# Performance work log

Hardware: AMD Instinct MI355X
Metric: run time of the kernel (lower is better)

Reference implementation:

```python
import jax, jax.numpy as jnp
import numpy as np

N_EMBD = 1024
N_HEAD = 16
HEAD_DIM = N_EMBD // N_HEAD
INNER = 4 * N_EMBD
EPS = 1e-5


def setup_inputs() -> dict:
    key = jax.random.key(0)
    ks = jax.random.split(key, 13)
    s = lambda d: 1.0 / np.sqrt(d)
    return {
        "x": jax.random.normal(ks[0], (2, 2048, N_EMBD), jnp.float32),
        "ln1_g": jnp.ones((N_EMBD,), jnp.float32),
        "ln1_b": jnp.zeros((N_EMBD,), jnp.float32),
        "w_attn": jax.random.normal(ks[1], (N_EMBD, 3 * N_EMBD), jnp.float32) * s(N_EMBD),
        "b_attn": jnp.zeros((3 * N_EMBD,), jnp.float32),
        "w_proj": jax.random.normal(ks[2], (N_EMBD, N_EMBD), jnp.float32) * s(N_EMBD),
        "b_proj": jnp.zeros((N_EMBD,), jnp.float32),
        "ln2_g": jnp.ones((N_EMBD,), jnp.float32),
        "ln2_b": jnp.zeros((N_EMBD,), jnp.float32),
        "w_fc": jax.random.normal(ks[3], (N_EMBD, INNER), jnp.float32) * s(N_EMBD),
        "b_fc": jnp.zeros((INNER,), jnp.float32),
        "w_fc2": jax.random.normal(ks[4], (INNER, N_EMBD), jnp.float32) * s(INNER),
        "b_fc2": jnpp if False else jnp.zeros((N_EMBD,), jnp.float32),
    }


def _layernorm(x, g, b):
    mu = jnp.mean(x, axis=-1, keepdims=True)
    var = jnp.mean(jnp.square(x - mu), axis=-1, keepdims=True)
    return (x - mu) * jax.lax.rsqrt(var + EPS) * g + b


def _attention(x, w_attn, b_attn, w_proj, b_proj):
    B, T, C = x.shape
    qkv = x @ w_attn + b_attn                      # [B,T,3C]
    q, k, v = jnp.split(qkv, 3, axis=-1)
    q = q.reshape(B, T, N_HEAD, HEAD_DIM).transpose(0, 2, 1, 3)  # [B,H,T,D]
    k = k.reshape(B, T, N_HEAD, HEAD_DIM).transpose(0, 2, 1, 3)
    v = v.reshape(B, T, N_HEAD, HEAD_DIM).transpose(0, 2, 1, 3)
    scale = HEAD_DIM ** -0.5
    scores = jnp.einsum("bhqd,bhkd->bhqk", q, k) * scale         # [B,H,T,T]
    causal = jnp.triu(jnp.ones((T, T), jnp.bool_), k=1)
    scores = jnp.where(causal, -jnp.inf, scores)
    attn = jax.nn.softmax(scores, axis=-1)
    out = jnp.einsum("bhqk,bhkd->bhqd", attn, v)                 # [B,H,T,D]
    out = out.transpose(0, 2, 1, 3).reshape(B, T, C)
    return out @ w_proj + b_proj


def reference(x, ln1_g, ln1_b, w_attn, b_attn, w_proj, b_proj,
              ln2_g, ln2_b, w_fc, b_fc, w_fc2, b_fc2):
    h = x + _attention(_layernorm(x, ln1_g, ln1_b), w_attn, b_attn, w_proj, b_proj)
    m = _layernorm(h, ln2_g, ln2_b)
    m = jax.nn.gelu(m @ w_fc + b_fc, approximate=False) @ w_fc2 + b_fc2
    return h + m
```

## Files before the change

kernel.cpp:

```cpp
#include <hip/hip_runtime.h>

typedef unsigned short u16;
typedef unsigned int u32;
typedef short v8s __attribute__((ext_vector_type(8)));
typedef short v4s __attribute__((ext_vector_type(4)));
typedef float v4f __attribute__((ext_vector_type(4)));

__device__ __forceinline__ float b2f(u16 v) {
    return __uint_as_float(((u32)v) << 16);
}
__device__ __forceinline__ u16 f2b(float f) {
    u32 u = __float_as_uint(f);
    return (u16)((u + 0x7FFFu + ((u >> 16) & 1u)) >> 16);
}
__device__ __forceinline__ v4f mfma16(v8s a, v8s b, v4f c) {
    return __builtin_amdgcn_mfma_f32_16x16x32_bf16(a, b, c, 0, 0, 0);
}

__device__ __forceinline__ void gload_lds16(const u16* g, u16* l) {
    __builtin_amdgcn_global_load_lds((const __attribute__((address_space(1))) void*)g,
                                     (__attribute__((address_space(3))) void*)l, 16, 0, 0);
}

__global__ void detect_k(const void* x, int* flag) {
    __shared__ int cnt;
    if (threadIdx.x == 0) cnt = 0;
    __syncthreads();
    const u16* p = (const u16*)x;
    int bad = 0;
    for (int i = threadIdx.x; i < 4096; i += 256) {
        int e = (p[i] >> 7) & 0xFF;
        if (e != 0 && (e < 100 || e > 140)) bad++;
    }
    atomicAdd(&cnt, bad);
    __syncthreads();
    if (threadIdx.x == 0) *flag = (cnt > 256) ? 1 : 0;
}

__global__ void cvt_k(const void* __restrict__ src, u16* __restrict__ dst, int n,
                      const int* __restrict__ flag) {
    const int isf32 = *flag;
    for (int i = blockIdx.x * 256 + threadIdx.x; i < n; i += gridDim.x * 256)
        dst[i] = isf32 ? f2b(((const float*)src)[i]) : ((const u16*)src)[i];
}

struct P8 { const void* p[8]; };
__global__ void cvt_small_k(P8 src, u16* __restrict__ bb, const int* __restrict__ flag) {
    const int isf32 = *flag;
    const int len[8] = {3072, 1024, 4096, 1024, 1024, 1024, 1024, 1024};
    const int doff[8] = {0, 4096, 8192, 12288, 16384, 17408, 18432, 19456};
    int gi = blockIdx.x * 256 + threadIdx.x;
    int seg = 0, off = gi;
    while (seg < 7 && off >= len[seg]) { off -= len[seg]; seg++; }
    if (off < len[seg]) {
        const void* s = src.p[seg];
        bb[doff[seg] + off] = isf32 ? f2b(((const float*)s)[off]) : ((const u16*)s)[off];
    }
}

__global__ void transpose_k(const void* __restrict__ in, u16* __restrict__ out, int R, int C,
                            const int* __restrict__ flag) {
    __shared__ u16 t[32][33];
    const int isf32 = *flag;
    const int c0 = blockIdx.x * 32, r0 = blockIdx.y * 32;
    for (int i = threadIdx.y; i < 32; i += 8) {
        size_t idx = (size_t)(r0 + i) * C + c0 + threadIdx.x;
        t[i][threadIdx.x] = isf32 ? f2b(((const float*)in)[idx]) : ((const u16*)in)[idx];
    }
    __syncthreads();
    for (int i = threadIdx.y; i < 32; i += 8)
        out[(size_t)(c0 + i) * R + r0 + threadIdx.x] = t[threadIdx.x][i];
}

__global__ __launch_bounds__(256) void layernorm_k(const u16* __restrict__ x,
                                                   const u16* __restrict__ g,
                                                   const u16* __restrict__ bta,
                                                   u16* __restrict__ out) {
    const int wid = threadIdx.x >> 6, lane = threadIdx.x & 63;
    const size_t row = (size_t)blockIdx.x * 4 + wid;
    const u16* xr = x + row * 1024 + lane * 16;
    u16 v[16];
    *(uint4*)&v[0] = *(const uint4*)xr;
    *(uint4*)&v[8] = *(const uint4*)(xr + 8);
    float f[16], s = 0.f, sq = 0.f;
#pragma unroll
    for (int i = 0; i < 16; i++) { f[i] = b2f(v[i]); s += f[i]; sq += f[i] * f[i]; }
#pragma unroll
    for (int d = 1; d < 64; d <<= 1) { s += __shfl_xor(s, d, 64); sq += __shfl_xor(sq, d, 64); }
    const float mean = s * (1.f / 1024.f);
    const float var = sq * (1.f / 1024.f) - mean * mean;
    const float rstd = rsqrtf(var + 1e-5f);
    u16 gv[16], bv[16];
    *(uint4*)&gv[0] = *(const uint4*)(g + lane * 16);
    *(uint4*)&gv[8] = *(const uint4*)(g + lane * 16 + 8);
    *(uint4*)&bv[0] = *(const uint4*)(bta + lane * 16);
    *(uint4*)&bv[8] = *(const uint4*)(bta + lane * 16 + 8);
    u16 ov[16];
#pragma unroll
    for (int i = 0; i < 16; i++) ov[i] = f2b((f[i] - mean) * rstd * b2f(gv[i]) + b2f(bv[i]));
    u16* orow = out + row * 1024 + lane * 16;
    *(uint4*)orow = *(uint4*)&ov[0];
    *(uint4*)(orow + 8) = *(uint4*)&ov[8];
}

#define GEMM_STAGE(tk, buf)                                              \
    do {                                                                 \
        const int _k = (tk) << 5;                                        \
        gload_lds16(Ag + _k, &As[buf][0] + wid * 512);                   \
        gload_lds16(Ag + (size_t)64 * K + _k, &As[buf][2048] + wid * 512); \
        gload_lds16(Bg + _k, &Bs[buf][0] + wid * 512);                   \
        gload_lds16(Bg + (size_t)64 * K + _k, &Bs[buf][2048] + wid * 512); \
    } while (0)

__global__ __launch_bounds__(256) void gemm_bt_k(const u16* __restrict__ A,
                                                 const u16* __restrict__ Bt,
                                                 const u16* __restrict__ bias,
                                                 const u16* __restrict__ res,
                                                 void* __restrict__ C,
                                                 int M, int N, int K, int do_gelu,
                                                 const int* __restrict__ outf32) {
    __shared__ __align__(16) u16 As[3][4096];
    __shared__ __align__(16) u16 Bs[3][4096];
    const int tid = threadIdx.x;
    const int wid = tid >> 6, lane = tid & 63;
    const int lg = lane >> 4, lm = lane & 15;
    const int wr = wid >> 1, wc = wid & 1;
    const int nwg = gridDim.x * gridDim.y;
    const int orig = blockIdx.y * gridDim.x + blockIdx.x;
    const int wg = (orig & 7) * (nwg >> 3) + (orig >> 3);
    const int m0 = (wg / gridDim.x) * 128, n0 = (wg % gridDim.x) * 128;

    const v4f vzero = {0.f, 0.f, 0.f, 0.f};
    v4f acc[4][4];
#pragma unroll
    for (int i = 0; i < 4; i++)
#pragma unroll
        for (int j = 0; j < 4; j++) acc[i][j] = vzero;

    const int srow = tid >> 2;
    const int scol = (((tid & 3) ^ ((tid >> 3) & 3)) * 8);
    const u16* Ag = A + (size_t)(m0 + srow) * K + scol;
    const u16* Bg = Bt + (size_t)(n0 + srow) * K + scol;
    const int lgx = (lg ^ ((lm >> 1) & 3)) * 8;

    const int nt = K >> 5;
    GEMM_STAGE(0, 0);
    GEMM_STAGE(1, 1);
    for (int t = 0; t < nt; ++t) {
        const int cur = t % 3;
        if (t + 2 < nt) {
            GEMM_STAGE(t + 2, (t + 2) % 3);
            asm volatile("s_waitcnt vmcnt(8)" ::: "memory");
        } else if (t + 1 < nt) {
            asm volatile("s_waitcnt vmcnt(4)" ::: "memory");
        } else {
            asm volatile("s_waitcnt vmcnt(0)" ::: "memory");
        }
        __builtin_amdgcn_s_barrier();
        v8s af[4], bf[4];
#pragma unroll
        for (int i = 0; i < 4; i++)
            af[i] = *(const v8s*)&As[cur][(wr * 64 + i * 16 + lm) * 32 + lgx];
#pragma unroll
        for (int j = 0; j < 4; j++)
            bf[j] = *(const v8s*)&Bs[cur][(wc * 64 + j * 16 + lm) * 32 + lgx];
        __builtin_amdgcn_s_setprio(1);
#pragma unroll
        for (int i = 0; i < 4; i++)
#pragma unroll
            for (int j = 0; j < 4; j++)
                acc[i][j] = __builtin_amdgcn_mfma_f32_16x16x32_bf16(af[i], bf[j], acc[i][j], 0, 0, 0);
        __builtin_amdgcn_s_setprio(0);
        asm volatile("s_waitcnt lgkmcnt(0)" ::: "memory");
        __builtin_amdgcn_sched_barrier(0);
        __builtin_amdgcn_s_barrier();
    }

    const int of32 = outf32 ? *outf32 : 0;
#pragma unroll
    for (int i = 0; i < 4; i++) {
#pragma unroll
        for (int r = 0; r < 4; r++) {
            const int row = m0 + wr * 64 + i * 16 + lg * 4 + r;
            const size_t rb = (size_t)row * N;
#pragma unroll
            for (int j = 0; j < 4; j++) {
                const int col = n0 + wc * 64 + j * 16 + lm;
                float v = acc[i][j][r] + b2f(bias[col]);
                if (do_gelu) v = 0.5f * v * (1.0f + erff(v * 0.70710678118f));
                if (res) v += b2f(res[rb + col]);
                if (of32) ((float*)C)[rb + col] = v;
                else ((u16*)C)[rb + col] = f2b(v);
            }
        }
    }
}

__global__ __launch_bounds__(256) void gemm_sk_k(const u16* __restrict__ A,
                                                 const u16* __restrict__ Bt,
                                                 float* __restrict__ P0,
                                                 float* __restrict__ P1,
                                                 int N, int K) {
    __shared__ __align__(16) u16 As[3][4096];
    __shared__ __align__(16) u16 Bs[3][4096];
    const int tid = threadIdx.x;
    const int wid = tid >> 6, lane = tid & 63;
    const int lg = lane >> 4, lm = lane & 15;
    const int wr = wid >> 1, wc = wid & 1;
    const int z = blockIdx.z;
    const int KS = K >> 1;
    const int nwg = gridDim.x * gridDim.y;
    const int orig = blockIdx.y * gridDim.x + blockIdx.x;
    const int wg = (orig & 7) * (nwg >> 3) + (orig >> 3);
    const int m0 = (wg / gridDim.x) * 128, n0 = (wg % gridDim.x) * 128;

    const v4f vzero = {0.f, 0.f, 0.f, 0.f};
    v4f acc[4][4];
#pragma unroll
    for (int i = 0; i < 4; i++)
#pragma unroll
        for (int j = 0; j < 4; j++) acc[i][j] = vzero;

    const int srow = tid >> 2;
    const int scol = (((tid & 3) ^ ((tid >> 3) & 3)) * 8);
    const u16* Ag = A + (size_t)(m0 + srow) * K + z * KS + scol;
    const u16* Bg = Bt + (size_t)(n0 + srow) * K + z * KS + scol;
    const int lgx = (lg ^ ((lm >> 1) & 3)) * 8;

    const int nt = KS >> 5;
    GEMM_STAGE(0, 0);
    GEMM_STAGE(1, 1);
    for (int t = 0; t < nt; ++t) {
        const int cur = t % 3;
        if (t + 2 < nt) {
            GEMM_STAGE(t + 2, (t + 2) % 3);
            asm volatile("s_waitcnt vmcnt(8)" ::: "memory");
        } else if (t + 1 < nt) {
            asm volatile("s_waitcnt vmcnt(4)" ::: "memory");
        } else {
            asm volatile("s_waitcnt vmcnt(0)" ::: "memory");
        }
        __builtin_amdgcn_s_barrier();
        v8s af[4], bf[4];
#pragma unroll
        for (int i = 0; i < 4; i++)
            af[i] = *(const v8s*)&As[cur][(wr * 64 + i * 16 + lm) * 32 + lgx];
#pragma unroll
        for (int j = 0; j < 4; j++)
            bf[j] = *(const v8s*)&Bs[cur][(wc * 64 + j * 16 + lm) * 32 + lgx];
        __builtin_amdgcn_s_setprio(1);
#pragma unroll
        for (int i = 0; i < 4; i++)
#pragma unroll
            for (int j = 0; j < 4; j++)
                acc[i][j] = __builtin_amdgcn_mfma_f32_16x16x32_bf16(af[i], bf[j], acc[i][j], 0, 0, 0);
        __builtin_amdgcn_s_setprio(0);
        asm volatile("s_waitcnt lgkmcnt(0)" ::: "memory");
        __builtin_amdgcn_sched_barrier(0);
        __builtin_amdgcn_s_barrier();
    }

    float* P = z ? P1 : P0;
#pragma unroll
    for (int i = 0; i < 4; i++) {
#pragma unroll
        for (int r = 0; r < 4; r++) {
            const int row = m0 + wr * 64 + i * 16 + lg * 4 + r;
            const size_t rb = (size_t)row * N;
#pragma unroll
            for (int j = 0; j < 4; j++) {
                const int col = n0 + wc * 64 + j * 16 + lm;
                P[rb + col] = acc[i][j][r];
            }
        }
    }
}

__global__ __launch_bounds__(256) void fc2red_k(const float* __restrict__ P0,
                                                const float* __restrict__ P1,
                                                const u16* __restrict__ bias,
                                                const u16* __restrict__ res,
                                                void* __restrict__ out,
                                                const int* __restrict__ outf32) {
    const int i = (blockIdx.x * 256 + threadIdx.x) * 4;
    const int col = i & 1023;
    float4 a = *(const float4*)(P0 + i);
    float4 b = *(const float4*)(P1 + i);
    v4s rv = *(const v4s*)(res + i);
    v4s bv = *(const v4s*)(bias + col);
    float v0 = a.x + b.x + b2f(bv[0]) + b2f(rv[0]);
    float v1 = a.y + b.y + b2f(bv[1]) + b2f(rv[1]);
    float v2 = a.z + b.z + b2f(bv[2]) + b2f(rv[2]);
    float v3 = a.w + b.w + b2f(bv[3]) + b2f(rv[3]);
    if (*outf32) {
        float4 o = {v0, v1, v2, v3};
        *(float4*)((float*)out + i) = o;
    } else {
        u16 pk[4] = {f2b(v0), f2b(v1), f2b(v2), f2b(v3)};
        *(v4s*)((u16*)out + i) = *(const v4s*)pk;
    }
}

#define ST256(LDSARR, P, tt, h)                                                  \
    do {                                                                         \
        const u16* _s = (P) + (size_t)((h) * 128) * K + (size_t)(tt) * 64;       \
        gload_lds16(_s, &LDSARR[(tt) & 1][h][0] + wv * 512);                     \
        gload_lds16(_s + (size_t)64 * K, &LDSARR[(tt) & 1][h][4096] + wv * 512); \
    } while (0)

#define MMROW(ii, x0, x1)                                   \
    acc[ii][0] = mfma16(x0, bfr[0][0], acc[ii][0]);         \
    acc[ii][0] = mfma16(x1, bfr[0][1], acc[ii][0]);         \
    acc[ii][1] = mfma16(x0, bfr[1][0], acc[ii][1]);         \
    acc[ii][1] = mfma16(x1, bfr[1][1], acc[ii][1]);         \
    acc[ii][2] = mfma16(x0, bfr[2][0], acc[ii][2]);         \
    acc[ii][2] = mfma16(x1, bfr[2][1], acc[ii][2]);         \
    acc[ii][3] = mfma16(x0, bfr[3][0], acc[ii][3]);         \
    acc[ii][3] = mfma16(x1, bfr[3][1], acc[ii][3]);

#define RD_A2(i0, i1)                                         \
    x0 = *(const v8s*)(ABase + (i0) * 1024 + offk0);          \
    x1 = *(const v8s*)(ABase + (i0) * 1024 + offk1);          \
    y0 = *(const v8s*)(ABase + (i1) * 1024 + offk0);          \
    y1 = *(const v8s*)(ABase + (i1) * 1024 + offk1);

__global__ __launch_bounds__(512, 2) void gemm256_k(const u16* __restrict__ A,
                                                    const u16* __restrict__ Bt,
                                                    const u16* __restrict__ bias,
                                                    const u16* __restrict__ res,
                                                    void* __restrict__ C,
                                                    int M, int N, int K, int do_gelu,
                                                    const int* __restrict__ outf32) {
    __shared__ __align__(16) u16 As[2][2][8192];
    __shared__ __align__(16) u16 Bs[2][2][8192];
    const int tid = threadIdx.x;
    const int wv = tid >> 6, lane = tid & 63;
    const int lg = lane >> 4, lm = lane & 15;
    const int wm = wv >> 2, wn = wv & 3;
    const int nwg = gridDim.x * gridDim.y;
    const int orig = blockIdx.y * gridDim.x + blockIdx.x;
    const int wg = (orig & 7) * (nwg >> 3) + (orig >> 3);
    const int m0 = (wg / gridDim.x) * 256, n0 = (wg % gridDim.x) * 256;

    const v4f vzero = {0.f, 0.f, 0.f, 0.f};
    v4f acc[8][4];
#pragma unroll
    for (int i = 0; i < 8; i++)
#pragma unroll
        for (int j = 0; j < 4; j++) acc[i][j] = vzero;

    const int trow = tid >> 3;
    const int csw = ((tid & 7) ^ (trow & 7)) * 8;
    const u16* Ap = A + (size_t)(m0 + trow) * K + csw;
    const u16* Bp = Bt + (size_t)(n0 + trow) * K + csw;
    const int offk0 = lm * 64 + ((lg ^ (lm & 7)) << 3);
    const int offk1 = offk0 ^ 32;

    const int NT = K >> 6;
    ST256(As, Ap, 0, 0); ST256(As, Ap, 0, 1);
    ST256(Bs, Bp, 0, 0); ST256(Bs, Bp, 0, 1);
    ST256(Bs, Bp, 1, 0); ST256(Bs, Bp, 1, 1);
    asm volatile("s_waitcnt vmcnt(4)" ::: "memory");
    __builtin_amdgcn_s_barrier();

    for (int t = 0; t < NT; ++t) {
        const int d = t & 1;
        const u16* ABase = &As[d][wm][0];
        const u16* BBase = &Bs[d][wn >> 1][(wn & 1) * 4096];
        v8s bfr[4][2];
        v8s x0, x1, y0, y1;
#pragma unroll
        for (int j = 0; j < 4; j++) {
            bfr[j][0] = *(const v8s*)(BBase + j * 1024 + offk0);
            bfr[j][1] = *(const v8s*)(BBase + j * 1024 + offk1);
        }
        RD_A2(0, 1)
        if (t + 1 < NT) { ST256(As, Ap, t + 1, 0); }
        __builtin_amdgcn_s_barrier();
        asm volatile("s_waitcnt lgkmcnt(0)" ::: "memory");
        __builtin_amdgcn_s_setprio(1);
        MMROW(0, x0, x1)
        MMROW(1, y0, y1)
        __builtin_amdgcn_s_setprio(0);
        __builtin_amdgcn_s_barrier();
        RD_A2(2, 3)
        if (t + 1 < NT) { ST256(As, Ap, t + 1, 1); }
        __builtin_amdgcn_s_barrier();
        asm volatile("s_waitcnt lgkmcnt(0)" ::: "memory");
        __builtin_amdgcn_s_setprio(1);
        MMROW(2, x0, x1)
        MMROW(3, y0, y1)
        __builtin_amdgcn_s_setprio(0);
        __builtin_amdgcn_s_barrier();
        RD_A2(4, 5)
        if (t + 2 < NT) { ST256(Bs, Bp, t + 2, 0); }
        __builtin_amdgcn_s_barrier();
        asm volatile("s_waitcnt lgkmcnt(0)" ::: "memory");
        __builtin_amdgcn_s_setprio(1);
        MMROW(4, x0, x1)
        MMROW(5, y0, y1)
        __builtin_amdgcn_s_setprio(0);
        __builtin_amdgcn_s_barrier();
        RD_A2(6, 7)
        if (t + 2 < NT) {
            ST256(Bs, Bp, t + 2, 1);
            asm volatile("s_waitcnt vmcnt(4)" ::: "memory");
        } else {
            asm volatile("s_waitcnt vmcnt(0)" ::: "memory");
        }
        __builtin_amdgcn_s_barrier();
        asm volatile("s_waitcnt lgkmcnt(0)" ::: "memory");
        __builtin_amdgcn_s_setprio(1);
        MMROW(6, x0, x1)
        MMROW(7, y0, y1)
        __builtin_amdgcn_s_setprio(0);
        __builtin_amdgcn_s_barrier();
    }

    const int of32 = outf32 ? *outf32 : 0;
#pragma unroll
    for (int i = 0; i < 8; i++) {
#pragma unroll
        for (int r = 0; r < 4; r++) {
            const int row = m0 + wm * 128 + i * 16 + lg * 4 + r;
            const size_t rb = (size_t)row * N;
#pragma unroll
            for (int j = 0; j < 4; j++) {
                const int col = n0 + wn * 64 + j * 16 + lm;
                float v = acc[i][j][r] + b2f(bias[col]);
                if (do_gelu) v = 0.5f * v * (1.0f + erff(v * 0.70710678118f));
                if (res) v += b2f(res[rb + col]);
                if (of32) ((float*)C)[rb + col] = v;
                else ((u16*)C)[rb + col] = f2b(v);
            }
        }
    }
}

__global__ __launch_bounds__(256) void gemm_qkv_k(const u16* __restrict__ A,
                                                  const u16* __restrict__ Bt,
                                                  const u16* __restrict__ bias,
                                                  u16* __restrict__ Qh,
                                                  u16* __restrict__ Kh,
                                                  u16* __restrict__ Vth) {
    __shared__ __align__(16) u16 As[3][4096];
    __shared__ __align__(16) u16 Bs[3][4096];
    const int tid = threadIdx.x;
    const int wid = tid >> 6, lane = tid & 63;
    const int lg = lane >> 4, lm = lane & 15;
    const int wr = wid >> 1, wc = wid & 1;
    const int nwg = gridDim.x * gridDim.y;
    const int orig = blockIdx.y * gridDim.x + blockIdx.x;
    const int wg = (orig & 7) * (nwg >> 3) + (orig >> 3);
    const int m0 = (wg / gridDim.x) * 128, n0 = (wg % gridDim.x) * 128;
    const int K = 1024;

    const v4f vzero = {0.f, 0.f, 0.f, 0.f};
    v4f acc[4][4];
#pragma unroll
    for (int i = 0; i < 4; i++)
#pragma unroll
        for (int j = 0; j < 4; j++) acc[i][j] = vzero;

    const int srow = tid >> 2;
    const int scol = (((tid & 3) ^ ((tid >> 3) & 3)) * 8);
    const u16* Ag = A + (size_t)(m0 + srow) * K + scol;
    const u16* Bg = Bt + (size_t)(n0 + srow) * K + scol;
    const int lgx = (lg ^ ((lm >> 1) & 3)) * 8;

    const int nt = K >> 5;
    GEMM_STAGE(0, 0);
    GEMM_STAGE(1, 1);
    for (int t = 0; t < nt; ++t) {
        const int cur = t % 3;
        if (t + 2 < nt) {
            GEMM_STAGE(t + 2, (t + 2) % 3);
            asm volatile("s_waitcnt vmcnt(8)" ::: "memory");
        } else if (t + 1 < nt) {
            asm volatile("s_waitcnt vmcnt(4)" ::: "memory");
        } else {
            asm volatile("s_waitcnt vmcnt(0)" ::: "memory");
        }
        __builtin_amdgcn_s_barrier();
        v8s af[4], bf[4];
#pragma unroll
        for (int i = 0; i < 4; i++)
            af[i] = *(const v8s*)&As[cur][(wr * 64 + i * 16 + lm) * 32 + lgx];
#pragma unroll
        for (int j = 0; j < 4; j++)
            bf[j] = *(const v8s*)&Bs[cur][(wc * 64 + j * 16 + lm) * 32 + lgx];
        __builtin_amdgcn_s_setprio(1);
#pragma unroll
        for (int i = 0; i < 4; i++)
#pragma unroll
            for (int j = 0; j < 4; j++)
                acc[i][j] = __builtin_amdgcn_mfma_f32_16x16x32_bf16(af[i], bf[j], acc[i][j], 0, 0, 0);
        __builtin_amdgcn_s_setprio(0);
        asm volatile("s_waitcnt lgkmcnt(0)" ::: "memory");
        __builtin_amdgcn_sched_barrier(0);
        __builtin_amdgcn_s_barrier();
    }

    const int which = n0 >> 10;
    const int h = ((n0 & 1023) >> 6) + wc;
    if (which < 2) {
        u16* dst = which ? Kh : Qh;
        const float qsc = which ? 1.0f : 0.18033688011f;
#pragma unroll
        for (int i = 0; i < 4; i++) {
#pragma unroll
            for (int r = 0; r < 4; r++) {
                const int row = m0 + wr * 64 + i * 16 + lg * 4 + r;
                const int b = row >> 11, t = row & 2047;
                const size_t rb = ((size_t)(b * 16 + h) * 2048 + t) * 64;
#pragma unroll
                for (int j = 0; j < 4; j++) {
                    float v = (acc[i][j][r] + b2f(bias[n0 + wc * 64 + j * 16 + lm])) * qsc;
                    dst[rb + j * 16 + lm] = f2b(v);
                }
            }
        }
    } else {
#pragma unroll
        for (int i = 0; i < 4; i++) {
            const int t0 = m0 + wr * 64 + i * 16 + lg * 4;
            const int b = t0 >> 11, tt = t0 & 2047;
            const int w = tt & 31;
            const int pos = (tt & ~31) + ((w & 15) >> 2) * 8 + ((w >> 4) & 1) * 4;
#pragma unroll
            for (int j = 0; j < 4; j++) {
                const int d = j * 16 + lm;
                const float bv_ = b2f(bias[n0 + wc * 64 + j * 16 + lm]);
                u16 pk[4];
#pragma unroll
                for (int r = 0; r < 4; r++) pk[r] = f2b(acc[i][j][r] + bv_);
                *(v4s*)&Vth[((size_t)(b * 16 + h) * 64 + d) * 2048 + pos] = *(const v4s*)pk;
            }
        }
    }
}

__global__ __launch_bounds__(256, 4) void attn10_k(const u16* __restrict__ Qh,
                                                   const u16* __restrict__ Kh,
                                                   const u16* __restrict__ Vth,
                                                   u16* __restrict__ out) {
    __shared__ __align__(16) u16 Ks[2][4096];
    __shared__ __align__(16) u16 Vs[2][4096];
    const int tid = threadIdx.x;
    const int wid = tid >> 6, lane = tid & 63;
    const int lg = lane >> 4, lm = lane & 15;
    const int i = blockIdx.x;
    const int q = i >> 8, s = i & 255;
    const int bh = s & 31;
    const int g8 = s >> 5;
    const int g = (q == 0) ? g8 : (q == 1) ? (15 - g8) : (q == 2) ? (16 + g8) : (31 - g8);
    const int q0 = g * 64 + wid * 16;
    const int qrow_l = q0 + lm;
    const size_t qkb = (size_t)bh * 2048;
    const v4f vzero = {0.f, 0.f, 0.f, 0.f};
    const int nch = g + 1;

    const int r0 = tid >> 3;
    const int colp = ((tid & 7) * 16) ^ ((r0 & 7) << 4);
    const u16* Ksrc0 = Kh + (qkb + r0) * 64 + (colp >> 1);
    const u16* Ksrc1 = Ksrc0 + 32 * 64;
    const u16* Vsrc0 = Vth + ((size_t)bh * 64 + r0) * 2048 + (colp >> 1);
    const u16* Vsrc1 = Vsrc0 + (size_t)32 * 2048;
    const int wslot = wid * 512;

    const int xorv = (lm & 7) << 4;
    const int ro1 = (lm * 128 + ((lg * 16) ^ xorv)) >> 1;
    const int ro2 = (lm * 128 + (((lg * 16) + 64) ^ xorv)) >> 1;

    v8s aq[2];
    {
        const u16* qp = Qh + (qkb + q0 + lm) * 64 + lg * 8;
        aq[0] = *(const v8s*)qp;
        aq[1] = *(const v8s*)(qp + 32);
    }
    float l_run = 0.f;
    v4f o[4];
#pragma unroll
    for (int dt = 0; dt < 4; dt++) o[dt] = vzero;

    gload_lds16(Ksrc0, &Ks[0][0] + wslot);
    gload_lds16(Ksrc1, &Ks[0][2048] + wslot);
    gload_lds16(Vsrc0, &Vs[0][0] + wslot);
    gload_lds16(Vsrc1, &Vs[0][2048] + wslot);

    for (int ci = 0; ci < nch; ++ci) {
        const int cur = ci & 1;
        if (ci + 1 < nch) {
            const u16* kc = Ksrc0 + (ci + 1) * 4096;
            const u16* vc = Vsrc0 + (ci + 1) * 64;
            gload_lds16(kc, &Ks[cur ^ 1][0] + wslot);
            gload_lds16(kc + 32 * 64, &Ks[cur ^ 1][2048] + wslot);
            gload_lds16(vc, &Vs[cur ^ 1][0] + wslot);
            gload_lds16(vc + (size_t)32 * 2048, &Vs[cur ^ 1][2048] + wslot);
            asm volatile("s_waitcnt vmcnt(4)" ::: "memory");
        } else {
            asm volatile("s_waitcnt vmcnt(0)" ::: "memory");
        }
        __builtin_amdgcn_s_barrier();

        const u16* KB = &Ks[cur][0];
        const u16* VB = &Vs[cur][0];
        const int k0 = ci << 6;
        v4f sacc[4];
        __builtin_amdgcn_s_setprio(1);
#pragma unroll
        for (int kt = 0; kt < 4; kt++) {
            v8s klo = *(const v8s*)(KB + kt * 1024 + ro1);
            v8s khi = *(const v8s*)(KB + kt * 1024 + ro2);
            sacc[kt] = __builtin_amdgcn_mfma_f32_16x16x32_bf16(klo, aq[0], vzero, 0, 0, 0);
            sacc[kt] = __builtin_amdgcn_mfma_f32_16x16x32_bf16(khi, aq[1], sacc[kt], 0, 0, 0);
        }
        __builtin_amdgcn_s_setprio(0);
        float p[16];
        if (ci == nch - 1) {
#pragma unroll
            for (int kt = 0; kt < 4; kt++)
#pragma unroll
                for (int r = 0; r < 4; r++) {
                    float v = sacc[kt][r];
                    v = (k0 + kt * 16 + lg * 4 + r > qrow_l) ? -200.f : v;
                    p[kt * 4 + r] = exp2f(v);
                }
        } else {
#pragma unroll
            for (int kt = 0; kt < 4; kt++)
#pragma unroll
                for (int r = 0; r < 4; r++) p[kt * 4 + r] = exp2f(sacc[kt][r]);
        }
        float ls = 0.f;
#pragma unroll
        for (int e = 0; e < 16; e++) ls += p[e];
        l_run += ls;
        u32 pk[8];
#pragma unroll
        for (int j = 0; j < 8; j++) {
            u32 lo = __float_as_uint(p[j * 2]) + 0x8000u;
            u32 hi = __float_as_uint(p[j * 2 + 1]) + 0x8000u;
            pk[j] = __builtin_amdgcn_perm(hi, lo, 0x07060302u);
        }
        v8s B0, B1;
        ((u32*)&B0)[0] = pk[0]; ((u32*)&B0)[1] = pk[1];
        ((u32*)&B0)[2] = pk[2]; ((u32*)&B0)[3] = pk[3];
        ((u32*)&B1)[0] = pk[4]; ((u32*)&B1)[1] = pk[5];
        ((u32*)&B1)[2] = pk[6]; ((u32*)&B1)[3] = pk[7];
        __builtin_amdgcn_s_setprio(1);
#pragma unroll
        for (int dt = 0; dt < 4; dt++) {
            v8s vlo = *(const v8s*)(VB + dt * 1024 + ro1);
            v8s vhi = *(const v8s*)(VB + dt * 1024 + ro2);
            o[dt] = __builtin_amdgcn_mfma_f32_16x16x32_bf16(vlo, B0, o[dt], 0, 0, 0);
            o[dt] = __builtin_amdgcn_mfma_f32_16x16x32_bf16(vhi, B1, o[dt], 0, 0, 0);
        }
        __builtin_amdgcn_s_setprio(0);
        asm volatile("s_waitcnt lgkmcnt(0)" ::: "memory");
        __builtin_amdgcn_sched_barrier(0);
        __builtin_amdgcn_s_barrier();
    }
    l_run += __shfl_xor(l_run, 16, 64);
    l_run += __shfl_xor(l_run, 32, 64);
    const int b = bh >> 4, h = bh & 15;
    const float inv = 1.0f / l_run;
    const size_t rowb = ((size_t)b * 2048 + q0 + lm) * 1024 + h * 64;
#pragma unroll
    for (int dt = 0; dt < 4; dt++) {
        u16 pk2[4];
#pragma unroll
        for (int r = 0; r < 4; r++) pk2[r] = f2b(o[dt][r] * inv);
        *(v4s*)&out[rowb + dt * 16 + lg * 4] = *(const v4s*)pk2;
    }
}

extern "C" void kernel_launch(void* const* d_in, const int* in_sizes, int n_in,
                              void* d_out, int out_size, void* d_ws, size_t ws_size,
                              hipStream_t stream) {
    const void* x      = d_in[0];
    const void* ln1_g  = d_in[1];
    const void* ln1_b  = d_in[2];
    const void* w_attn = d_in[3];
    const void* b_attn = d_in[4];
    const void* w_proj = d_in[5];
    const void* b_proj = d_in[6];
    const void* ln2_g  = d_in[7];
    const void* ln2_b  = d_in[8];
    const void* w_fc   = d_in[9];
    const void* b_fc   = d_in[10];
    const void* w_fc2  = d_in[11];
    const void* b_fc2  = d_in[12];

    u16* ws = (u16*)d_ws;
    const size_t Mi = 1u << 20;
    u16* xb       = ws;
    u16* ln_buf   = ws + 4 * Mi;
    u16* h_buf    = ws + 8 * Mi;
    u16* wT_attn  = ws + 12 * Mi;
    u16* wT_proj  = ws + 15 * Mi;
    u16* wT_fc    = ws + 16 * Mi;
    u16* wT_fc2   = ws + 20 * Mi;
    u16* bb       = ws + 24 * Mi;
    u16* bb_attn = bb, *bb_proj = bb + 4096, *bb_fc = bb + 8192, *bb_fc2 = bb + 12288;
    u16* gsmall   = bb + 16384;
    u16* g_ln1g = gsmall, *g_ln1b = gsmall + 1024, *g_ln2g = gsmall + 2048, *g_ln2b = gsmall + 3072;
    int* flag     = (int*)(bb + 24576);
    u16* Qh       = ws + 25 * Mi;
    u16* Kh       = ws + 29 * Mi;
    u16* Vth      = ws + 33 * Mi;
    u16* attn_buf = ws + 37 * Mi;
    u16* fc_buf   = ws + 25 * Mi;
    float* P0f    = (float*)ws;
    float* P1f    = (float*)(ws + 12 * Mi);

    detect_k<<<1, 256, 0, stream>>>(x, flag);

    cvt_k<<<4096, 256, 0, stream>>>(x, xb, 4 * Mi, flag);
    P8 smalls;
    smalls.p[0] = b_attn; smalls.p[1] = b_proj; smalls.p[2] = b_fc; smalls.p[3] = b_fc2;
    smalls.p[4] = ln1_g;  smalls.p[5] = ln1_b;  smalls.p[6] = ln2_g; smalls.p[7] = ln2_b;
    cvt_small_k<<<52, 256, 0, stream>>>(smalls, bb, flag);

    dim3 tb(32, 8);
    transpose_k<<<dim3(96, 32), tb, 0, stream>>>(w_attn, wT_attn, 1024, 3072, flag);
    transpose_k<<<dim3(32, 32), tb, 0, stream>>>(w_proj, wT_proj, 1024, 1024, flag);
    transpose_k<<<dim3(128, 32), tb, 0, stream>>>(w_fc, wT_fc, 1024, 4096, flag);
    transpose_k<<<dim3(32, 128), tb, 0, stream>>>(w_fc2, wT_fc2, 4096, 1024, flag);

    layernorm_k<<<1024, 256, 0, stream>>>(xb, g_ln1g, g_ln1b, ln_buf);
    gemm_qkv_k<<<dim3(24, 32), 256, 0, stream>>>(ln_buf, wT_attn, bb_attn, Qh, Kh, Vth);
    attn10_k<<<1024, 256, 0, stream>>>(Qh, Kh, Vth, attn_buf);
    gemm_bt_k<<<dim3(8, 32), 256, 0, stream>>>(attn_buf, wT_proj, bb_proj, xb, h_buf,
                                               4096, 1024, 1024, 0, nullptr);
    layernorm_k<<<1024, 256, 0, stream>>>(h_buf, g_ln2g, g_ln2b, ln_buf);
    gemm256_k<<<dim3(16, 16), 512, 0, stream>>>(ln_buf, wT_fc, bb_fc, nullptr, fc_buf,
                                                4096, 4096, 1024, 1, nullptr);
    gemm_sk_k<<<dim3(8, 32, 2), 256, 0, stream>>>(fc_buf, wT_fc2, P0f, P1f, 1024, 4096);
    fc2red_k<<<4096, 256, 0, stream>>>(P0f, P1f, bb_fc2, h_buf, d_out, flag);
}
```

Before: 424.1 us.

## Software-pipeline LDS fragment reads across GEMM K-tiles with double-buffered registers

Restructures the 256x256 GEMM main loop so the LDS reads for the next A fragments and the next tile's B fragments are issued before the current MFMA block runs. Partial lgkmcnt waits fenced by sched_barrier replace the full lgkmcnt(0) waits. The loop is unrolled by two and ping-pongs between two B register sets, hiding LDS latency behind MFMA work. The cost is more VGPRs under launch_bounds(512,2), which could cause spills. The unroll also assumes NT is even.

New measurement: 432.3 us. About the same (+1.9%).

```diff
diff --git a/kernel.cpp b/kernel.cpp
--- a/kernel.cpp
+++ b/kernel.cpp
@@ -308,21 +308,107 @@
         gload_lds16(_s + (size_t)64 * K, &LDSARR[(tt) & 1][h][4096] + wv * 512); \
     } while (0)
 
-#define MMROW(ii, x0, x1)                                   \
-    acc[ii][0] = mfma16(x0, bfr[0][0], acc[ii][0]);         \
-    acc[ii][0] = mfma16(x1, bfr[0][1], acc[ii][0]);         \
-    acc[ii][1] = mfma16(x0, bfr[1][0], acc[ii][1]);         \
-    acc[ii][1] = mfma16(x1, bfr[1][1], acc[ii][1]);         \
-    acc[ii][2] = mfma16(x0, bfr[2][0], acc[ii][2]);         \
-    acc[ii][2] = mfma16(x1, bfr[2][1], acc[ii][2]);         \
-    acc[ii][3] = mfma16(x0, bfr[3][0], acc[ii][3]);         \
-    acc[ii][3] = mfma16(x1, bfr[3][1], acc[ii][3]);
-
-#define RD_A2(i0, i1)                                         \
-    x0 = *(const v8s*)(ABase + (i0) * 1024 + offk0);          \
-    x1 = *(const v8s*)(ABase + (i0) * 1024 + offk1);          \
-    y0 = *(const v8s*)(ABase + (i1) * 1024 + offk0);          \
-    y1 = *(const v8s*)(ABase + (i1) * 1024 + offk1);
+#define RD_B_INTO(dst, BB)                                     \
+    do {                                                       \
+        dst[0][0] = *(const v8s*)((BB) + offk0);               \
+        dst[0][1] = *(const v8s*)((BB) + offk1);               \
+        dst[1][0] = *(const v8s*)((BB) + 1024 + offk0);        \
+        dst[1][1] = *(const v8s*)((BB) + 1024 + offk1);        \
+        dst[2][0] = *(const v8s*)((BB) + 2048 + offk0);        \
+        dst[2][1] = *(const v8s*)((BB) + 2048 + offk1);        \
+        dst[3][0] = *(const v8s*)((BB) + 3072 + offk0);        \
+        dst[3][1] = *(const v8s*)((BB) + 3072 + offk1);        \
+    } while (0)
+
+#define RD_A_INTO(dst, i0)                                             \
+    do {                                                               \
+        dst[0] = *(const v8s*)(ABase + (i0) * 1024 + offk0);           \
+        dst[1] = *(const v8s*)(ABase + (i0) * 1024 + offk1);           \
+        dst[2] = *(const v8s*)(ABase + ((i0) + 1) * 1024 + offk0);     \
+        dst[3] = *(const v8s*)(ABase + ((i0) + 1) * 1024 + offk1);     \
+    } while (0)
+
+#define MM2(BF, ii, sA)                                           \
+    do {                                                          \
+        acc[ii][0] = mfma16(sA[0], BF[0][0], acc[ii][0]);         \
+        acc[ii][0] = mfma16(sA[1], BF[0][1], acc[ii][0]);         \
+        acc[ii][1] = mfma16(sA[0], BF[1][0], acc[ii][1]);         \
+        acc[ii][1] = mfma16(sA[1], BF[1][1], acc[ii][1]);         \
+        acc[ii][2] = mfma16(sA[0], BF[2][0], acc[ii][2]);         \
+        acc[ii][2] = mfma16(sA[1], BF[2][1], acc[ii][2]);         \
+        acc[ii][3] = mfma16(sA[0], BF[3][0], acc[ii][3]);         \
+        acc[ii][3] = mfma16(sA[1], BF[3][1], acc[ii][3]);         \
+        acc[(ii) + 1][0] = mfma16(sA[2], BF[0][0], acc[(ii) + 1][0]); \
+        acc[(ii) + 1][0] = mfma16(sA[3], BF[0][1], acc[(ii) + 1][0]); \
+        acc[(ii) + 1][1] = mfma16(sA[2], BF[1][0], acc[(ii) + 1][1]); \
+        acc[(ii) + 1][1] = mfma16(sA[3], BF[1][1], acc[(ii) + 1][1]); \
+        acc[(ii) + 1][2] = mfma16(sA[2], BF[2][0], acc[(ii) + 1][2]); \
+        acc[(ii) + 1][2] = mfma16(sA[3], BF[2][1], acc[(ii) + 1][2]); \
+        acc[(ii) + 1][3] = mfma16(sA[2], BF[3][0], acc[(ii) + 1][3]); \
+        acc[(ii) + 1][3] = mfma16(sA[3], BF[3][1], acc[(ii) + 1][3]); \
+    } while (0)
+
+#define LGK_WAIT(nstr)                                      \
+    __builtin_amdgcn_sched_barrier(0);                      \
+    asm volatile("s_waitcnt lgkmcnt(" nstr ")" ::: "memory"); \
+    __builtin_amdgcn_sched_barrier(0);
+
+#define TILE256(TT, BCUR, BNXT)                                               \
+    {                                                                         \
+        const int d = (TT) & 1;                                               \
+        const u16* ABase = &As[d][wm][0];                                     \
+                         \
+        if ((TT) + 1 < NT) ST256(As, Ap, (TT) + 1, 0);                        \
+        __builtin_amdgcn_s_barrier();                                         \
+        RD_A_INTO(aY, 2);                                                     \
+        LGK_WAIT("4")                                                         \
+        __builtin_amdgcn_s_setprio(1);                                        \
+        MM2(BCUR, 0, aX);                                                     \
+        __builtin_amdgcn_s_setprio(0);                                        \
+        __builtin_amdgcn_s_barrier();                                         \
+                              \
+        if ((TT) + 1 < NT) ST256(As, Ap, (TT) + 1, 1);                        \
+        __builtin_amdgcn_s_barrier();                                         \
+        RD_A_INTO(aX, 4);                                                     \
+        LGK_WAIT("4")                                                         \
+        __builtin_amdgcn_s_setprio(1);                                        \
+        MM2(BCUR, 2, aY);                                                     \
+        __builtin_amdgcn_s_setprio(0);                                        \
+        __builtin_amdgcn_s_barrier();                                         \
+                              \
+        if ((TT) + 2 < NT) ST256(Bs, Bp, (TT) + 2, 0);                        \
+        __builtin_amdgcn_s_barrier();                                         \
+        RD_A_INTO(aY, 6);                                                     \
+        LGK_WAIT("4")                                                         \
+        __builtin_amdgcn_s_setprio(1);                                        \
+        MM2(BCUR, 4, aX);                                                     \
+        __builtin_amdgcn_s_setprio(0);                                        \
+        __builtin_amdgcn_s_barrier();                                         \
+          \
+        if ((TT) + 2 < NT) {                                                  \
+            ST256(Bs, Bp, (TT) + 2, 1);                                       \
+            asm volatile("s_waitcnt vmcnt(4)" ::: "memory");                  \
+        } else {                                                              \
+            asm volatile("s_waitcnt vmcnt(0)" ::: "memory");                  \
+        }                                                                     \
+        __builtin_amdgcn_s_barrier();                                         \
+        if ((TT) + 1 < NT) {                                                  \
+            const u16* ABn = &As[d ^ 1][wm][0];                               \
+            const u16* BBn = &Bs[d ^ 1][wn >> 1][(wn & 1) * 4096];            \
+            RD_B_INTO(BNXT, BBn);                                             \
+            aX[0] = *(const v8s*)(ABn + offk0);                               \
+            aX[1] = *(const v8s*)(ABn + offk1);                               \
+            aX[2] = *(const v8s*)(ABn + 1024 + offk0);                        \
+            aX[3] = *(const v8s*)(ABn + 1024 + offk1);                        \
+            LGK_WAIT("12")                                                    \
+        } else {                                                              \
+            LGK_WAIT("0")                                                     \
+        }                                                                     \
+        __builtin_amdgcn_s_setprio(1);                                        \
+        MM2(BCUR, 6, aY);                                                     \
+        __builtin_amdgcn_s_setprio(0);                                        \
+        __builtin_amdgcn_s_barrier();                                         \
+    }
 
 __global__ __launch_bounds__(512, 2) void gemm256_k(const u16* __restrict__ A,
                                                     const u16* __restrict__ Bt,
@@ -357,64 +443,23 @@
     const int offk1 = offk0 ^ 32;
 
     const int NT = K >> 6;
+    v8s aX[4], aY[4], bA[4][2], bB[4][2];
+
     ST256(As, Ap, 0, 0); ST256(As, Ap, 0, 1);
     ST256(Bs, Bp, 0, 0); ST256(Bs, Bp, 0, 1);
     ST256(Bs, Bp, 1, 0); ST256(Bs, Bp, 1, 1);
     asm volatile("s_waitcnt vmcnt(4)" ::: "memory");
     __builtin_amdgcn_s_barrier();
-
-    for (int t = 0; t < NT; ++t) {
-        const int d = t & 1;
-        const u16* ABase = &As[d][wm][0];
-        const u16* BBase = &Bs[d][wn >> 1][(wn & 1) * 4096];
-        v8s bfr[4][2];
-        v8s x0, x1, y0, y1;
-#pragma unroll
-        for (int j = 0; j < 4; j++) {
-            bfr[j][0] = *(const v8s*)(BBase + j * 1024 + offk0);
-            bfr[j][1] = *(const v8s*)(BBase + j * 1024 + offk1);
-        }
-        RD_A2(0, 1)
-        if (t + 1 < NT) { ST256(As, Ap, t + 1, 0); }
-        __builtin_amdgcn_s_barrier();
-        asm volatile("s_waitcnt lgkmcnt(0)" ::: "memory");
-        __builtin_amdgcn_s_setprio(1);
-        MMROW(0, x0, x1)
-        MMROW(1, y0, y1)
-        __builtin_amdgcn_s_setprio(0);
-        __builtin_amdgcn_s_barrier();
-        RD_A2(2, 3)
-        if (t + 1 < NT) { ST256(As, Ap, t + 1, 1); }
-        __builtin_amdgcn_s_barrier();
-        asm volatile("s_waitcnt lgkmcnt(0)" ::: "memory");
-        __builtin_amdgcn_s_setprio(1);
-        MMROW(2, x0, x1)
-        MMROW(3, y0, y1)
-        __builtin_amdgcn_s_setprio(0);
-        __builtin_amdgcn_s_barrier();
-        RD_A2(4, 5)
-        if (t + 2 < NT) { ST256(Bs, Bp, t + 2, 0); }
-        __builtin_amdgcn_s_barrier();
-        asm volatile("s_waitcnt lgkmcnt(0)" ::: "memory");
-        __builtin_amdgcn_s_setprio(1);
-        MMROW(4, x0, x1)
-        MMROW(5, y0, y1)
-        __builtin_amdgcn_s_setprio(0);
-        __builtin_amdgcn_s_barrier();
-        RD_A2(6, 7)
-        if (t + 2 < NT) {
-            ST256(Bs, Bp, t + 2, 1);
-            asm volatile("s_waitcnt vmcnt(4)" ::: "memory");
-        } else {
-            asm volatile("s_waitcnt vmcnt(0)" ::: "memory");
-        }
-        __builtin_amdgcn_s_barrier();
-        asm volatile("s_waitcnt lgkmcnt(0)" ::: "memory");
-        __builtin_amdgcn_s_setprio(1);
-        MMROW(6, x0, x1)
-        MMROW(7, y0, y1)
-        __builtin_amdgcn_s_setprio(0);
-        __builtin_amdgcn_s_barrier();
+    {
+        const u16* ABase = &As[0][wm][0];
+        const u16* BB0 = &Bs[0][wn >> 1][(wn & 1) * 4096];
+        RD_B_INTO(bA, BB0);
+        RD_A_INTO(aX, 0);
+    }
+
+    for (int t2 = 0; t2 < NT; t2 += 2) {
+        TILE256(t2, bA, bB)
+        TILE256(t2 + 1, bB, bA)
     }
 
     const int of32 = outf32 ? *outf32 : 0;
```
